# Kernel tuning notes

Hardware: AMD Instinct MI355X
Metric: run time of the kernel (lower is better)

The kernel has to match this reference:

```python
import jax, jax.numpy as jnp
import numpy as np

HIDDEN = 1024
INTER = 4096
N_EXPERTS = 8
TOP_K = 2


def setup_inputs() -> dict:
    key = jax.random.key(0)
    ks = jax.random.split(key, 5)
    B, S = 2, 1024
    scale_h = 1.0 / np.sqrt(HIDDEN)
    scale_i = 1.0 / np.sqrt(INTER)
    return {
        "hidden_states": jax.random.normal(ks[0], (B, S, HIDDEN), dtype=jnp.float32),
        "router_w": jax.random.normal(ks[1], (N_EXPERTS, HIDDEN), dtype=jnp.float32) * scale_h,
        "gate_w": jax.random.normal(ks[2], (N_EXPERTS, INTER, HIDDEN), dtype=jnp.float32) * scale_h,
        "up_w": jax.random.normal(ks[3], (N_EXPERTS, INTER, HIDDEN), dtype=jnp.float32) * scale_h,
        "down_w": jax.random.normal(ks[4], (N_EXPERTS, HIDDEN, INTER), dtype=jnp.float32) * scale_i,
        "top_k": TOP_K,
    }


def reference(hidden_states, router_w, gate_w, up_w, down_w, top_k):
    B, S, D = hidden_states.shape
    E = router_w.shape[0]
    x = hidden_states.reshape(-1, D)              # [T, D]
    T = x.shape[0]

    router_logits = x @ router_w.T                # [T, E]
    probs = jax.nn.softmax(router_logits.astype(jnp.float32), axis=-1)
    routing_weights, selected = jax.lax.top_k(probs, top_k)   # [T, k]
    routing_weights = routing_weights.astype(x.dtype)

    # Dense combine weights: w[t, e] = routing weight if expert e selected for token t else 0
    combine = jnp.zeros((T, E), x.dtype).at[jnp.arange(T)[:, None], selected].add(routing_weights)

    # SwiGLU expert MLPs, computed for all experts then combined (same math as gather/scatter loop)
    g = jnp.einsum('td,ehd->eth', x, gate_w)      # [E, T, H]
    u = jnp.einsum('td,ehd->eth', x, up_w)        # [E, T, H]
    h = jax.nn.silu(g) * u
    expert_out = jnp.einsum('eth,edh->etd', h, down_w)  # [E, T, D]
    out = jnp.einsum('etd,te->td', expert_out, combine)  # [T, D]

    return out.reshape(B, S, D), router_logits
```

## Files before the change

### kernel.cpp

```cpp
#include <hip/hip_runtime.h>
#include <hip/hip_bf16.h>

#define HIDDEN 1024
#define INTER 4096
#define NEXP 8
#define T_TOK 2048

typedef short bf16x8 __attribute__((ext_vector_type(8)));
typedef float f32x4 __attribute__((ext_vector_type(4)));

#define CHUNK(row, kq) ((unsigned int)((row) * 64u + ((((unsigned int)(kq)) ^ ((((unsigned int)(row)) >> 1) & 3u)) << 4)))

__device__ __forceinline__ unsigned short f2bf(float f) {
    union { float f; unsigned int u; } v; v.f = f;
    return (unsigned short)(v.u >> 16);
}

__device__ __forceinline__ uint4 pack8trunc(float4 a, float4 b) {
    union { float4 f; unsigned short s[8]; } x, y; x.f = a; y.f = b;
    uint4 r;
    r.x = (unsigned int)x.s[1] | ((unsigned int)x.s[3] << 16);
    r.y = (unsigned int)x.s[5] | ((unsigned int)x.s[7] << 16);
    r.z = (unsigned int)y.s[1] | ((unsigned int)y.s[3] << 16);
    r.w = (unsigned int)y.s[5] | ((unsigned int)y.s[7] << 16);
    return r;
}

__device__ __forceinline__ void block_sync() {
    asm volatile("s_waitcnt lgkmcnt(0)" ::: "memory");
    __builtin_amdgcn_s_barrier();
    asm volatile("" ::: "memory");
}

__global__ void router_kernel(const float* __restrict__ x,
                              const float* __restrict__ rw,
                              float* __restrict__ logits_out,
                              int* __restrict__ counts,
                              int* __restrict__ ids,
                              float* __restrict__ wts,
                              int* __restrict__ tsel) {
    int t = blockIdx.x * 4 + (threadIdx.x >> 6);
    int lane = threadIdx.x & 63;
    if (t >= T_TOK) return;
    const float4* xr = (const float4*)(x + (size_t)t * HIDDEN);
    float acc[NEXP];
#pragma unroll
    for (int e = 0; e < NEXP; e++) acc[e] = 0.f;
#pragma unroll
    for (int c = 0; c < 4; c++) {
        float4 xv = xr[lane + c * 64];
#pragma unroll
        for (int e = 0; e < NEXP; e++) {
            float4 wv = ((const float4*)(rw + (size_t)e * HIDDEN))[lane + c * 64];
            acc[e] += xv.x * wv.x + xv.y * wv.y + xv.z * wv.z + xv.w * wv.w;
        }
    }
#pragma unroll
    for (int e = 0; e < NEXP; e++) {
        float v = acc[e];
        for (int off = 32; off >= 1; off >>= 1) v += __shfl_xor(v, off, 64);
        acc[e] = v;
    }
    if (lane == 0) {
        float* lo = logits_out + (size_t)t * NEXP;
        float mx = acc[0];
#pragma unroll
        for (int e = 1; e < NEXP; e++) mx = fmaxf(mx, acc[e]);
        float p[NEXP], s = 0.f;
#pragma unroll
        for (int e = 0; e < NEXP; e++) { p[e] = __expf(acc[e] - mx); s += p[e]; }
        float inv = 1.f / s;
#pragma unroll
        for (int e = 0; e < NEXP; e++) { p[e] *= inv; lo[e] = acc[e]; }
        int i1 = 0;
#pragma unroll
        for (int e = 1; e < NEXP; e++) if (p[e] > p[i1]) i1 = e;
        int i2 = (i1 == 0) ? 1 : 0;
#pragma unroll
        for (int e = 0; e < NEXP; e++) if (e != i1 && e != i2 && p[e] > p[i2]) i2 = e;
        int s1 = atomicAdd(&counts[i1], 1);
        ids[i1 * T_TOK + s1] = t; wts[i1 * T_TOK + s1] = p[i1];
        int s2 = atomicAdd(&counts[i2], 1);
        ids[i2 * T_TOK + s2] = t; wts[i2 * T_TOK + s2] = p[i2];
        tsel[t * 2]     = i1 * T_TOK + s1;
        tsel[t * 2 + 1] = i2 * T_TOK + s2;
    }
}

__global__ void scan_kernel(const int* __restrict__ counts, int* __restrict__ offsets) {
    if (threadIdx.x == 0) {
        int s = 0;
        for (int e = 0; e < NEXP; e++) { offsets[e] = s; s += counts[e]; }
    }
}

__global__ __launch_bounds__(1024) void gemm_gu(
    const float* __restrict__ x, const float* __restrict__ gw, const float* __restrict__ uw,
    const int* __restrict__ counts, const int* __restrict__ offsets,
    const int* __restrict__ ids, unsigned short* __restrict__ h) {
    const int e = blockIdx.z;
    const int cnt = counts[e];
    const int mt = blockIdx.y;
    if (mt * 256 >= cnt) return;
    const int nt = blockIdx.x;
    const int tid = threadIdx.x;
    const int lane = tid & 63, wid = tid >> 6;
    const int wm = wid >> 2, wn = wid & 3;

    __shared__ __align__(16) char lds[65536];

    const int arow = tid >> 2, akq = tid & 3;
    int ali = mt * 256 + arow; if (ali >= cnt) ali = cnt - 1;
    const unsigned int aoff = (unsigned int)(ids[e * T_TOK + ali] * HIDDEN + akq * 8);
    const unsigned int wAo = CHUNK(arow, akq);
    const int bsel = tid >> 9;
    const int bi = tid & 511;
    const int brow = bi >> 2, bkq = bi & 3;
    const float* bsrc = (bsel ? uw : gw) + (size_t)e * INTER * HIDDEN
                        + (size_t)(nt * 128 + brow) * HIDDEN + bkq * 8;
    const unsigned int wBo = 16384u + ((unsigned int)bsel << 13) + CHUNK(brow, bkq);

    f32x4 accg[4][2], accu[4][2];
#pragma unroll
    for (int mf = 0; mf < 4; mf++)
#pragma unroll
        for (int nf = 0; nf < 2; nf++)
#pragma unroll
            for (int v = 0; v < 4; v++) { accg[mf][nf][v] = 0.f; accu[mf][nf][v] = 0.f; }

    float4 a0, a1, b0, b1;
    a0 = *(const float4*)(x + aoff); a1 = *(const float4*)(x + aoff + 4);
    b0 = *(const float4*)(bsrc);     b1 = *(const float4*)(bsrc + 4);

    for (int kt = 0; kt < 32; kt++) {
        const unsigned int bb = (unsigned int)(kt & 1) << 15;
        *(uint4*)(lds + bb + wAo) = pack8trunc(a0, a1);
        *(uint4*)(lds + bb + wBo) = pack8trunc(b0, b1);
        if (kt < 31) {
            const int ko = (kt + 1) * 32;
            a0 = *(const float4*)(x + aoff + ko); a1 = *(const float4*)(x + aoff + ko + 4);
            b0 = *(const float4*)(bsrc + ko);     b1 = *(const float4*)(bsrc + ko + 4);
        }
        block_sync();
        const unsigned int kqr = (unsigned int)(lane >> 4);
        const unsigned int rl = (unsigned int)(lane & 15);
        bf16x8 a[4];
#pragma unroll
        for (int mf = 0; mf < 4; mf++)
            a[mf] = *(const bf16x8*)(lds + bb + CHUNK(wm * 64 + mf * 16 + rl, kqr));
#pragma unroll
        for (int nf = 0; nf < 2; nf++) {
            const unsigned int br = wn * 32 + nf * 16 + rl;
            bf16x8 bg = *(const bf16x8*)(lds + bb + 16384 + CHUNK(br, kqr));
            bf16x8 bu = *(const bf16x8*)(lds + bb + 24576 + CHUNK(br, kqr));
#pragma unroll
            for (int mf = 0; mf < 4; mf++) {
                accg[mf][nf] = __builtin_amdgcn_mfma_f32_16x16x32_bf16(a[mf], bg, accg[mf][nf], 0, 0, 0);
                accu[mf][nf] = __builtin_amdgcn_mfma_f32_16x16x32_bf16(a[mf], bu, accu[mf][nf], 0, 0, 0);
            }
        }
    }

    const int hoff = offsets[e];
#pragma unroll
    for (int mf = 0; mf < 4; mf++)
#pragma unroll
        for (int v = 0; v < 4; v++) {
            int il = wm * 64 + mf * 16 + ((lane >> 4) << 2) + v;
            int i = mt * 256 + il;
            if (i < cnt) {
                size_t rowbase = (size_t)(hoff + i) * INTER + nt * 128 + wn * 32 + (lane & 15);
#pragma unroll
                for (int nf = 0; nf < 2; nf++) {
                    float g = accg[mf][nf][v], u = accu[mf][nf][v];
                    float sg = g / (1.f + __expf(-g));
                    h[rowbase + nf * 16] = f2bf(sg * u);
                }
            }
        }
}

__global__ __launch_bounds__(512) void gemm_down(
    const unsigned short* __restrict__ h, const float* __restrict__ dw,
    const int* __restrict__ counts, const int* __restrict__ offsets,
    const float* __restrict__ wts, float* __restrict__ y) {
    const int ez = blockIdx.z;
    const int e = ez >> 1, ksp = ez & 1;
    const int cnt = counts[e];
    const int mt = blockIdx.y;
    if (mt * 128 >= cnt) return;
    const int nt = blockIdx.x;
    const int tid = threadIdx.x;
    const int lane = tid & 63, wid = tid >> 6;
    const int wm = wid >> 2, wn = wid & 3;

    __shared__ __align__(16) char lds[32768];

    const int hoff = offsets[e];
    const float* dbase = dw + (size_t)e * HIDDEN * INTER;

    const int row = tid >> 2, kq = tid & 3;
    int li = mt * 128 + row; if (li >= cnt) li = cnt - 1;
    const unsigned int aoff = (unsigned int)((hoff + li) * INTER + ksp * 2048 + kq * 8);
    const unsigned int wAo = CHUNK(row, kq);
    const unsigned int boff = (unsigned int)((nt * 128 + row) * INTER + ksp * 2048 + kq * 8);
    const unsigned int wBo = 8192u + CHUNK(row, kq);

    f32x4 acc[4][2];
#pragma unroll
    for (int mf = 0; mf < 4; mf++)
#pragma unroll
        for (int nf = 0; nf < 2; nf++)
#pragma unroll
            for (int v = 0; v < 4; v++) acc[mf][nf][v] = 0.f;

    int4 av; float4 b0, b1;
    av = *(const int4*)(h + aoff);
    b0 = *(const float4*)(dbase + boff); b1 = *(const float4*)(dbase + boff + 4);

    for (int kt = 0; kt < 64; kt++) {
        const unsigned int bb = (unsigned int)(kt & 1) << 14;
        *(int4*)(lds + bb + wAo) = av;
        *(uint4*)(lds + bb + wBo) = pack8trunc(b0, b1);
        if (kt < 63) {
            const int ko = (kt + 1) * 32;
            av = *(const int4*)(h + aoff + ko);
            b0 = *(const float4*)(dbase + boff + ko); b1 = *(const float4*)(dbase + boff + ko + 4);
        }
        block_sync();
        const unsigned int kqr = (unsigned int)(lane >> 4);
        const unsigned int rl = (unsigned int)(lane & 15);
        bf16x8 a[4];
#pragma unroll
        for (int mf = 0; mf < 4; mf++)
            a[mf] = *(const bf16x8*)(lds + bb + CHUNK(wm * 64 + mf * 16 + rl, kqr));
#pragma unroll
        for (int nf = 0; nf < 2; nf++) {
            bf16x8 b = *(const bf16x8*)(lds + bb + 8192 + CHUNK(wn * 32 + nf * 16 + rl, kqr));
#pragma unroll
            for (int mf = 0; mf < 4; mf++)
                acc[mf][nf] = __builtin_amdgcn_mfma_f32_16x16x32_bf16(a[mf], b, acc[mf][nf], 0, 0, 0);
        }
    }

#pragma unroll
    for (int mf = 0; mf < 4; mf++)
#pragma unroll
        for (int v = 0; v < 4; v++) {
            int il = wm * 64 + mf * 16 + ((lane >> 4) << 2) + v;
            int i = mt * 128 + il;
            if (i < cnt) {
                float w = wts[e * T_TOK + i];
                float* yrow = y + ((size_t)ksp * 4096 + hoff + i) * HIDDEN
                                + nt * 128 + wn * 32 + (lane & 15);
#pragma unroll
                for (int nf = 0; nf < 2; nf++)
                    yrow[nf * 16] = w * acc[mf][nf][v];
            }
        }
}

__global__ __launch_bounds__(256) void combine_kernel(
    const float* __restrict__ y, const int* __restrict__ offsets,
    const int* __restrict__ tsel, float* __restrict__ out) {
    const int t = blockIdx.x;
    const int d = threadIdx.x * 4;
    int p0 = tsel[t * 2], p1 = tsel[t * 2 + 1];
    size_t g0 = (size_t)(offsets[p0 >> 11] + (p0 & (T_TOK - 1)));
    size_t g1 = (size_t)(offsets[p1 >> 11] + (p1 & (T_TOK - 1)));
    float4 a0 = *(const float4*)(y + g0 * HIDDEN + d);
    float4 a1 = *(const float4*)(y + (4096 + g0) * HIDDEN + d);
    float4 b0 = *(const float4*)(y + g1 * HIDDEN + d);
    float4 b1 = *(const float4*)(y + (4096 + g1) * HIDDEN + d);
    float4 o;
    o.x = (a0.x + a1.x) + (b0.x + b1.x);
    o.y = (a0.y + a1.y) + (b0.y + b1.y);
    o.z = (a0.z + a1.z) + (b0.z + b1.z);
    o.w = (a0.w + a1.w) + (b0.w + b1.w);
    *(float4*)(out + (size_t)t * HIDDEN + d) = o;
}

extern "C" void kernel_launch(void* const* d_in, const int* in_sizes, int n_in,
                              void* d_out, int out_size, void* d_ws, size_t ws_size,
                              hipStream_t stream) {
    const float* x  = (const float*)d_in[0];
    const float* rw = (const float*)d_in[1];
    const float* gw = (const float*)d_in[2];
    const float* uw = (const float*)d_in[3];
    const float* dw = (const float*)d_in[4];
    float* out = (float*)d_out;
    float* logits = out + (size_t)T_TOK * HIDDEN;

    char* ws = (char*)d_ws;
    int*   counts  = (int*)ws;
    int*   offsets = (int*)(ws + 32);
    int*   tsel    = (int*)(ws + 1024);
    int*   ids     = (int*)(ws + 20480);
    float* wts     = (float*)(ws + 90112);
    unsigned short* h = (unsigned short*)(ws + 262144);
    float* y       = (float*)(ws + 262144 + 33554432);

    hipMemsetAsync(counts, 0, 8 * sizeof(int), stream);

    router_kernel<<<T_TOK / 4, 256, 0, stream>>>(x, rw, logits, counts, ids, wts, tsel);
    scan_kernel<<<1, 64, 0, stream>>>(counts, offsets);
    gemm_gu<<<dim3(INTER / 128, 8, NEXP), 1024, 0, stream>>>(x, gw, uw, counts, offsets, ids, h);
    gemm_down<<<dim3(HIDDEN / 128, 16, NEXP * 2), 512, 0, stream>>>(h, dw, counts, offsets, wts, y);
    combine_kernel<<<T_TOK, 256, 0, stream>>>(y, offsets, tsel, out);
}
```

Before: 295.0 us.

## Restructure GEMM main loops into two-stage prefetch pipeline with split LDS buffers

Both the gate/up and down GEMM loops now stage the next tile into the alternate LDS buffer while computing on the current one, and prefetch global data two tiles ahead. The loop is unrolled by two with separate even/odd shared buffers, so buffer addresses are static. This is meant to hide global load latency and LDS write cost behind MFMA work. The barrier count per iteration stays at one. Register pressure rises somewhat and the extra prologue adds complexity.

```diff
diff --git a/kernel.cpp b/kernel.cpp
--- a/kernel.cpp
+++ b/kernel.cpp
@@ -107,7 +107,8 @@
     const int lane = tid & 63, wid = tid >> 6;
     const int wm = wid >> 2, wn = wid & 3;
 
-    __shared__ __align__(16) char lds[65536];
+    __shared__ __align__(16) char bufE[32768];
+    __shared__ __align__(16) char bufO[32768];
 
     const int arow = tid >> 2, akq = tid & 3;
     int ali = mt * 256 + arow; if (ali >= cnt) ali = cnt - 1;
@@ -128,38 +129,52 @@
 #pragma unroll
             for (int v = 0; v < 4; v++) { accg[mf][nf][v] = 0.f; accu[mf][nf][v] = 0.f; }
 
-    float4 a0, a1, b0, b1;
-    a0 = *(const float4*)(x + aoff); a1 = *(const float4*)(x + aoff + 4);
-    b0 = *(const float4*)(bsrc);     b1 = *(const float4*)(bsrc + 4);
-
-    for (int kt = 0; kt < 32; kt++) {
-        const unsigned int bb = (unsigned int)(kt & 1) << 15;
-        *(uint4*)(lds + bb + wAo) = pack8trunc(a0, a1);
-        *(uint4*)(lds + bb + wBo) = pack8trunc(b0, b1);
-        if (kt < 31) {
-            const int ko = (kt + 1) * 32;
-            a0 = *(const float4*)(x + aoff + ko); a1 = *(const float4*)(x + aoff + ko + 4);
-            b0 = *(const float4*)(bsrc + ko);     b1 = *(const float4*)(bsrc + ko + 4);
-        }
-        block_sync();
-        const unsigned int kqr = (unsigned int)(lane >> 4);
-        const unsigned int rl = (unsigned int)(lane & 15);
-        bf16x8 a[4];
-#pragma unroll
-        for (int mf = 0; mf < 4; mf++)
-            a[mf] = *(const bf16x8*)(lds + bb + CHUNK(wm * 64 + mf * 16 + rl, kqr));
-#pragma unroll
-        for (int nf = 0; nf < 2; nf++) {
-            const unsigned int br = wn * 32 + nf * 16 + rl;
-            bf16x8 bg = *(const bf16x8*)(lds + bb + 16384 + CHUNK(br, kqr));
-            bf16x8 bu = *(const bf16x8*)(lds + bb + 24576 + CHUNK(br, kqr));
-#pragma unroll
-            for (int mf = 0; mf < 4; mf++) {
-                accg[mf][nf] = __builtin_amdgcn_mfma_f32_16x16x32_bf16(a[mf], bg, accg[mf][nf], 0, 0, 0);
-                accu[mf][nf] = __builtin_amdgcn_mfma_f32_16x16x32_bf16(a[mf], bu, accu[mf][nf], 0, 0, 0);
-            }
-        }
-    }
+    float4 s0, s1, t0, t1;
+    s0 = *(const float4*)(x + aoff); s1 = *(const float4*)(x + aoff + 4);
+    t0 = *(const float4*)(bsrc);     t1 = *(const float4*)(bsrc + 4);
+    *(uint4*)(bufE + wAo) = pack8trunc(s0, s1);
+    *(uint4*)(bufE + wBo) = pack8trunc(t0, t1);
+    s0 = *(const float4*)(x + aoff + 32); s1 = *(const float4*)(x + aoff + 36);
+    t0 = *(const float4*)(bsrc + 32);     t1 = *(const float4*)(bsrc + 36);
+    block_sync();
+
+    const unsigned int kqr = (unsigned int)(lane >> 4);
+    const unsigned int rl = (unsigned int)(lane & 15);
+
+#define GU_BODY(KT, RB, WB)                                                             \
+    {                                                                                   \
+        bf16x8 fa[4];                                                                   \
+        _Pragma("unroll")                                                               \
+        for (int mf = 0; mf < 4; mf++)                                                  \
+            fa[mf] = *(const bf16x8*)((RB) + CHUNK(wm * 64 + mf * 16 + rl, kqr));       \
+        if ((KT) + 1 < 32) {                                                            \
+            *(uint4*)((WB) + wAo) = pack8trunc(s0, s1);                                 \
+            *(uint4*)((WB) + wBo) = pack8trunc(t0, t1);                                 \
+        }                                                                               \
+        if ((KT) + 2 < 32) {                                                            \
+            const int ko = ((KT) + 2) * 32;                                             \
+            s0 = *(const float4*)(x + aoff + ko); s1 = *(const float4*)(x + aoff + ko + 4); \
+            t0 = *(const float4*)(bsrc + ko);     t1 = *(const float4*)(bsrc + ko + 4); \
+        }                                                                               \
+        _Pragma("unroll")                                                               \
+        for (int nf = 0; nf < 2; nf++) {                                                \
+            const unsigned int br = wn * 32 + nf * 16 + rl;                             \
+            bf16x8 bg = *(const bf16x8*)((RB) + 16384 + CHUNK(br, kqr));                \
+            bf16x8 bu = *(const bf16x8*)((RB) + 24576 + CHUNK(br, kqr));                \
+            _Pragma("unroll")                                                           \
+            for (int mf = 0; mf < 4; mf++) {                                            \
+                accg[mf][nf] = __builtin_amdgcn_mfma_f32_16x16x32_bf16(fa[mf], bg, accg[mf][nf], 0, 0, 0); \
+                accu[mf][nf] = __builtin_amdgcn_mfma_f32_16x16x32_bf16(fa[mf], bu, accu[mf][nf], 0, 0, 0); \
+            }                                                                           \
+        }                                                                               \
+        block_sync();                                                                   \
+    }
+
+    for (int kt = 0; kt < 32; kt += 2) {
+        GU_BODY(kt, bufE, bufO)
+        GU_BODY(kt + 1, bufO, bufE)
+    }
+#undef GU_BODY
 
     const int hoff = offsets[e];
 #pragma unroll
@@ -194,7 +209,8 @@
     const int lane = tid & 63, wid = tid >> 6;
     const int wm = wid >> 2, wn = wid & 3;
 
-    __shared__ __align__(16) char lds[32768];
+    __shared__ __align__(16) char bufE[16384];
+    __shared__ __align__(16) char bufO[16384];
 
     const int hoff = offsets[e];
     const float* dbase = dw + (size_t)e * HIDDEN * INTER;
@@ -217,31 +233,45 @@
     int4 av; float4 b0, b1;
     av = *(const int4*)(h + aoff);
     b0 = *(const float4*)(dbase + boff); b1 = *(const float4*)(dbase + boff + 4);
-
-    for (int kt = 0; kt < 64; kt++) {
-        const unsigned int bb = (unsigned int)(kt & 1) << 14;
-        *(int4*)(lds + bb + wAo) = av;
-        *(uint4*)(lds + bb + wBo) = pack8trunc(b0, b1);
-        if (kt < 63) {
-            const int ko = (kt + 1) * 32;
-            av = *(const int4*)(h + aoff + ko);
-            b0 = *(const float4*)(dbase + boff + ko); b1 = *(const float4*)(dbase + boff + ko + 4);
-        }
-        block_sync();
-        const unsigned int kqr = (unsigned int)(lane >> 4);
-        const unsigned int rl = (unsigned int)(lane & 15);
-        bf16x8 a[4];
-#pragma unroll
-        for (int mf = 0; mf < 4; mf++)
-            a[mf] = *(const bf16x8*)(lds + bb + CHUNK(wm * 64 + mf * 16 + rl, kqr));
-#pragma unroll
-        for (int nf = 0; nf < 2; nf++) {
-            bf16x8 b = *(const bf16x8*)(lds + bb + 8192 + CHUNK(wn * 32 + nf * 16 + rl, kqr));
-#pragma unroll
-            for (int mf = 0; mf < 4; mf++)
-                acc[mf][nf] = __builtin_amdgcn_mfma_f32_16x16x32_bf16(a[mf], b, acc[mf][nf], 0, 0, 0);
-        }
-    }
+    *(int4*)(bufE + wAo) = av;
+    *(uint4*)(bufE + wBo) = pack8trunc(b0, b1);
+    av = *(const int4*)(h + aoff + 32);
+    b0 = *(const float4*)(dbase + boff + 32); b1 = *(const float4*)(dbase + boff + 36);
+    block_sync();
+
+    const unsigned int kqr = (unsigned int)(lane >> 4);
+    const unsigned int rl = (unsigned int)(lane & 15);
+
+#define DN_BODY(KT, RB, WB)                                                             \
+    {                                                                                   \
+        bf16x8 fa[4];                                                                   \
+        _Pragma("unroll")                                                               \
+        for (int mf = 0; mf < 4; mf++)                                                  \
+            fa[mf] = *(const bf16x8*)((RB) + CHUNK(wm * 64 + mf * 16 + rl, kqr));       \
+        if ((KT) + 1 < 64) {                                                            \
+            *(int4*)((WB) + wAo) = av;                                                  \
+            *(uint4*)((WB) + wBo) = pack8trunc(b0, b1);                                 \
+        }                                                                               \
+        if ((KT) + 2 < 64) {                                                            \
+            const int ko = ((KT) + 2) * 32;                                             \
+            av = *(const int4*)(h + aoff + ko);                                         \
+            b0 = *(const float4*)(dbase + boff + ko); b1 = *(const float4*)(dbase + boff + ko + 4); \
+        }                                                                               \
+        _Pragma("unroll")                                                               \
+        for (int nf = 0; nf < 2; nf++) {                                                \
+            bf16x8 b = *(const bf16x8*)((RB) + 8192 + CHUNK(wn * 32 + nf * 16 + rl, kqr)); \
+            _Pragma("unroll")                                                           \
+            for (int mf = 0; mf < 4; mf++)                                              \
+                acc[mf][nf] = __builtin_amdgcn_mfma_f32_16x16x32_bf16(fa[mf], b, acc[mf][nf], 0, 0, 0); \
+        }                                                                               \
+        block_sync();                                                                   \
+    }
+
+    for (int kt = 0; kt < 64; kt += 2) {
+        DN_BODY(kt, bufE, bufO)
+        DN_BODY(kt + 1, bufO, bufE)
+    }
+#undef DN_BODY
 
 #pragma unroll
     for (int mf = 0; mf < 4; mf++)
```

Result: no change. 294.2 us (-0.3%).

## Restructure gate/up GEMM into 512-thread, BK=64 four-phase pipelined mainloop

Applied to the files above, without the earlier changes.

The gate/up expert GEMM drops from 1024 to 512 threads. Each wave now covers 128 rows (8 M-fragments), and the K step grows from 32 to 64, held in a 128 KB double-buffered LDS with an XOR swizzle over 8 chunks. Each K tile is split into four phases that interleave LDS fragment reads, stores of the next tile, and global prefetch two phases ahead, with s_setprio raised around the MFMA bursts. The aim is to hide global-load latency and cut barrier and LDS overhead per MFMA, at the cost of more accumulator registers and much more LDS, which limits occupancy to one block per CU.

```diff
diff --git a/kernel.cpp b/kernel.cpp
--- a/kernel.cpp
+++ b/kernel.cpp
@@ -30,6 +30,16 @@
     asm volatile("s_waitcnt lgkmcnt(0)" ::: "memory");
     __builtin_amdgcn_s_barrier();
     asm volatile("" ::: "memory");
+}
+__device__ __forceinline__ void bar() {
+    asm volatile("" ::: "memory");
+    __builtin_amdgcn_s_barrier();
+    asm volatile("" ::: "memory");
+}
+__device__ __forceinline__ void bar_lgkm0() {
+    asm volatile("" ::: "memory");
+    __builtin_amdgcn_s_barrier();
+    asm volatile("s_waitcnt lgkmcnt(0)" ::: "memory");
 }
 
 __global__ void router_kernel(const float* __restrict__ x,
@@ -94,7 +104,7 @@
     }
 }
 
-__global__ __launch_bounds__(1024) void gemm_gu(
+__global__ __launch_bounds__(512) void gemm_gu(
     const float* __restrict__ x, const float* __restrict__ gw, const float* __restrict__ uw,
     const int* __restrict__ counts, const int* __restrict__ offsets,
     const int* __restrict__ ids, unsigned short* __restrict__ h) {
@@ -107,66 +117,161 @@
     const int lane = tid & 63, wid = tid >> 6;
     const int wm = wid >> 2, wn = wid & 3;
 
-    __shared__ __align__(16) char lds[65536];
-
-    const int arow = tid >> 2, akq = tid & 3;
-    int ali = mt * 256 + arow; if (ali >= cnt) ali = cnt - 1;
-    const unsigned int aoff = (unsigned int)(ids[e * T_TOK + ali] * HIDDEN + akq * 8);
-    const unsigned int wAo = CHUNK(arow, akq);
-    const int bsel = tid >> 9;
-    const int bi = tid & 511;
-    const int brow = bi >> 2, bkq = bi & 3;
-    const float* bsrc = (bsel ? uw : gw) + (size_t)e * INTER * HIDDEN
-                        + (size_t)(nt * 128 + brow) * HIDDEN + bkq * 8;
-    const unsigned int wBo = 16384u + ((unsigned int)bsel << 13) + CHUNK(brow, bkq);
-
-    f32x4 accg[4][2], accu[4][2];
-#pragma unroll
-    for (int mf = 0; mf < 4; mf++)
+    __shared__ __align__(16) char lds[131072];
+
+    const float* gbase = gw + (size_t)e * INTER * HIDDEN;
+    const float* ubase = uw + (size_t)e * INTER * HIDDEN;
+
+    const int r0 = tid >> 3;
+    const int kq = tid & 7;
+    unsigned int aoffs0, aoffs1, aoffs2, aoffs3;
+    {
+        int li, row;
+        row = r0;        li = mt * 256 + row; if (li >= cnt) li = cnt - 1;
+        aoffs0 = (unsigned int)(ids[e * T_TOK + li] * HIDDEN + kq * 8);
+        row = r0 + 64;   li = mt * 256 + row; if (li >= cnt) li = cnt - 1;
+        aoffs1 = (unsigned int)(ids[e * T_TOK + li] * HIDDEN + kq * 8);
+        row = r0 + 128;  li = mt * 256 + row; if (li >= cnt) li = cnt - 1;
+        aoffs2 = (unsigned int)(ids[e * T_TOK + li] * HIDDEN + kq * 8);
+        row = r0 + 192;  li = mt * 256 + row; if (li >= cnt) li = cnt - 1;
+        aoffs3 = (unsigned int)(ids[e * T_TOK + li] * HIDDEN + kq * 8);
+    }
+    const unsigned int boff0 = (unsigned int)((nt * 128 + r0) * HIDDEN + kq * 8);
+    const unsigned int boff1 = (unsigned int)((nt * 128 + r0 + 64) * HIDDEN + kq * 8);
+    const unsigned int kqs = (unsigned int)((kq ^ (r0 & 7)) << 4);
+    const unsigned int wA0 = (unsigned int)r0 * 128u + kqs;
+    const unsigned int wB0 = (unsigned int)r0 * 128u + kqs;
+
+    const unsigned int rl  = (unsigned int)(lane & 15);
+    const unsigned int kqr = (unsigned int)(lane >> 4);
+    const unsigned int fx  = rl & 7u;
+    const unsigned int aro = ((unsigned int)wm * 128u + rl) * 128u;
+    const unsigned int bro = ((unsigned int)wn * 32u + rl) * 128u;
+    const unsigned int kx0 = ((0u * 4u + kqr) ^ fx) << 4;
+    const unsigned int kx1 = ((1u * 4u + kqr) ^ fx) << 4;
+
+    f32x4 accg[8][2], accu[8][2];
+#pragma unroll
+    for (int mf = 0; mf < 8; mf++)
 #pragma unroll
         for (int nf = 0; nf < 2; nf++)
 #pragma unroll
             for (int v = 0; v < 4; v++) { accg[mf][nf][v] = 0.f; accu[mf][nf][v] = 0.f; }
 
-    float4 a0, a1, b0, b1;
-    a0 = *(const float4*)(x + aoff); a1 = *(const float4*)(x + aoff + 4);
-    b0 = *(const float4*)(bsrc);     b1 = *(const float4*)(bsrc + 4);
-
-    for (int kt = 0; kt < 32; kt++) {
-        const unsigned int bb = (unsigned int)(kt & 1) << 15;
-        *(uint4*)(lds + bb + wAo) = pack8trunc(a0, a1);
-        *(uint4*)(lds + bb + wBo) = pack8trunc(b0, b1);
-        if (kt < 31) {
-            const int ko = (kt + 1) * 32;
-            a0 = *(const float4*)(x + aoff + ko); a1 = *(const float4*)(x + aoff + ko + 4);
-            b0 = *(const float4*)(bsrc + ko);     b1 = *(const float4*)(bsrc + ko + 4);
-        }
-        block_sync();
-        const unsigned int kqr = (unsigned int)(lane >> 4);
-        const unsigned int rl = (unsigned int)(lane & 15);
-        bf16x8 a[4];
-#pragma unroll
-        for (int mf = 0; mf < 4; mf++)
-            a[mf] = *(const bf16x8*)(lds + bb + CHUNK(wm * 64 + mf * 16 + rl, kqr));
-#pragma unroll
-        for (int nf = 0; nf < 2; nf++) {
-            const unsigned int br = wn * 32 + nf * 16 + rl;
-            bf16x8 bg = *(const bf16x8*)(lds + bb + 16384 + CHUNK(br, kqr));
-            bf16x8 bu = *(const bf16x8*)(lds + bb + 24576 + CHUNK(br, kqr));
-#pragma unroll
-            for (int mf = 0; mf < 4; mf++) {
-                accg[mf][nf] = __builtin_amdgcn_mfma_f32_16x16x32_bf16(a[mf], bg, accg[mf][nf], 0, 0, 0);
-                accu[mf][nf] = __builtin_amdgcn_mfma_f32_16x16x32_bf16(a[mf], bu, accu[mf][nf], 0, 0, 0);
-            }
-        }
-    }
+    float4 s0a, s0b, s0c, s0d, s1a, s1b, s1c, s1d;
+
+    {
+        float4 pa, pb, pc, pd;
+        pa = *(const float4*)(x + aoffs0); pb = *(const float4*)(x + aoffs0 + 4);
+        pc = *(const float4*)(x + aoffs1); pd = *(const float4*)(x + aoffs1 + 4);
+        *(uint4*)(lds + wA0)         = pack8trunc(pa, pb);
+        *(uint4*)(lds + wA0 + 8192)  = pack8trunc(pc, pd);
+        pa = *(const float4*)(x + aoffs2); pb = *(const float4*)(x + aoffs2 + 4);
+        pc = *(const float4*)(x + aoffs3); pd = *(const float4*)(x + aoffs3 + 4);
+        *(uint4*)(lds + wA0 + 16384) = pack8trunc(pa, pb);
+        *(uint4*)(lds + wA0 + 24576) = pack8trunc(pc, pd);
+        pa = *(const float4*)(gbase + boff0); pb = *(const float4*)(gbase + boff0 + 4);
+        pc = *(const float4*)(gbase + boff1); pd = *(const float4*)(gbase + boff1 + 4);
+        *(uint4*)(lds + 32768 + wB0)        = pack8trunc(pa, pb);
+        *(uint4*)(lds + 32768 + wB0 + 8192) = pack8trunc(pc, pd);
+        pa = *(const float4*)(ubase + boff0); pb = *(const float4*)(ubase + boff0 + 4);
+        pc = *(const float4*)(ubase + boff1); pd = *(const float4*)(ubase + boff1 + 4);
+        *(uint4*)(lds + 49152 + wB0)        = pack8trunc(pa, pb);
+        *(uint4*)(lds + 49152 + wB0 + 8192) = pack8trunc(pc, pd);
+    }
+    s0a = *(const float4*)(x + aoffs0 + 64); s0b = *(const float4*)(x + aoffs0 + 68);
+    s0c = *(const float4*)(x + aoffs1 + 64); s0d = *(const float4*)(x + aoffs1 + 68);
+    s1a = *(const float4*)(x + aoffs2 + 64); s1b = *(const float4*)(x + aoffs2 + 68);
+    s1c = *(const float4*)(x + aoffs3 + 64); s1d = *(const float4*)(x + aoffs3 + 68);
+    block_sync();
+
+#define GU_MFMA16(HH, FA0, FA1, FA2, FA3)                                                    \
+    accg[(HH)*4+0][0] = __builtin_amdgcn_mfma_f32_16x16x32_bf16(FA0, bg0, accg[(HH)*4+0][0], 0, 0, 0); \
+    accg[(HH)*4+0][1] = __builtin_amdgcn_mfma_f32_16x16x32_bf16(FA0, bg1, accg[(HH)*4+0][1], 0, 0, 0); \
+    accu[(HH)*4+0][0] = __builtin_amdgcn_mfma_f32_16x16x32_bf16(FA0, bu0, accu[(HH)*4+0][0], 0, 0, 0); \
+    accu[(HH)*4+0][1] = __builtin_amdgcn_mfma_f32_16x16x32_bf16(FA0, bu1, accu[(HH)*4+0][1], 0, 0, 0); \
+    accg[(HH)*4+1][0] = __builtin_amdgcn_mfma_f32_16x16x32_bf16(FA1, bg0, accg[(HH)*4+1][0], 0, 0, 0); \
+    accg[(HH)*4+1][1] = __builtin_amdgcn_mfma_f32_16x16x32_bf16(FA1, bg1, accg[(HH)*4+1][1], 0, 0, 0); \
+    accu[(HH)*4+1][0] = __builtin_amdgcn_mfma_f32_16x16x32_bf16(FA1, bu0, accu[(HH)*4+1][0], 0, 0, 0); \
+    accu[(HH)*4+1][1] = __builtin_amdgcn_mfma_f32_16x16x32_bf16(FA1, bu1, accu[(HH)*4+1][1], 0, 0, 0); \
+    accg[(HH)*4+2][0] = __builtin_amdgcn_mfma_f32_16x16x32_bf16(FA2, bg0, accg[(HH)*4+2][0], 0, 0, 0); \
+    accg[(HH)*4+2][1] = __builtin_amdgcn_mfma_f32_16x16x32_bf16(FA2, bg1, accg[(HH)*4+2][1], 0, 0, 0); \
+    accu[(HH)*4+2][0] = __builtin_amdgcn_mfma_f32_16x16x32_bf16(FA2, bu0, accu[(HH)*4+2][0], 0, 0, 0); \
+    accu[(HH)*4+2][1] = __builtin_amdgcn_mfma_f32_16x16x32_bf16(FA2, bu1, accu[(HH)*4+2][1], 0, 0, 0); \
+    accg[(HH)*4+3][0] = __builtin_amdgcn_mfma_f32_16x16x32_bf16(FA3, bg0, accg[(HH)*4+3][0], 0, 0, 0); \
+    accg[(HH)*4+3][1] = __builtin_amdgcn_mfma_f32_16x16x32_bf16(FA3, bg1, accg[(HH)*4+3][1], 0, 0, 0); \
+    accu[(HH)*4+3][0] = __builtin_amdgcn_mfma_f32_16x16x32_bf16(FA3, bu0, accu[(HH)*4+3][0], 0, 0, 0); \
+    accu[(HH)*4+3][1] = __builtin_amdgcn_mfma_f32_16x16x32_bf16(FA3, bu1, accu[(HH)*4+3][1], 0, 0, 0);
+
+#define GU_PHASE(T, P, CB, NB, SA, SB, SC, SD)                                               \
+    {                                                                                        \
+        const unsigned int kxs = ((P) & 1) ? kx1 : kx0;                                      \
+        bf16x8 fa0 = *(const bf16x8*)(lds + (CB) + aro + (((P)>>1)*4+0)*2048 + kxs);         \
+        bf16x8 fa1 = *(const bf16x8*)(lds + (CB) + aro + (((P)>>1)*4+1)*2048 + kxs);         \
+        bf16x8 fa2 = *(const bf16x8*)(lds + (CB) + aro + (((P)>>1)*4+2)*2048 + kxs);         \
+        bf16x8 fa3 = *(const bf16x8*)(lds + (CB) + aro + (((P)>>1)*4+3)*2048 + kxs);         \
+        bf16x8 bg0 = *(const bf16x8*)(lds + (CB) + 32768 + bro + 0*2048 + kxs);              \
+        bf16x8 bg1 = *(const bf16x8*)(lds + (CB) + 32768 + bro + 1*2048 + kxs);              \
+        bf16x8 bu0 = *(const bf16x8*)(lds + (CB) + 49152 + bro + 0*2048 + kxs);              \
+        bf16x8 bu1 = *(const bf16x8*)(lds + (CB) + 49152 + bro + 1*2048 + kxs);              \
+        if ((T) < 15) {                                                                      \
+            if ((P) == 0) {                                                                  \
+                *(uint4*)(lds + (NB) + wA0)        = pack8trunc(SA, SB);                     \
+                *(uint4*)(lds + (NB) + wA0 + 8192) = pack8trunc(SC, SD);                     \
+            } else if ((P) == 1) {                                                           \
+                *(uint4*)(lds + (NB) + wA0 + 16384) = pack8trunc(SA, SB);                    \
+                *(uint4*)(lds + (NB) + wA0 + 24576) = pack8trunc(SC, SD);                    \
+            } else if ((P) == 2) {                                                           \
+                *(uint4*)(lds + (NB) + 32768 + wB0)        = pack8trunc(SA, SB);             \
+                *(uint4*)(lds + (NB) + 32768 + wB0 + 8192) = pack8trunc(SC, SD);             \
+            } else {                                                                         \
+                *(uint4*)(lds + (NB) + 49152 + wB0)        = pack8trunc(SA, SB);             \
+                *(uint4*)(lds + (NB) + 49152 + wB0 + 8192) = pack8trunc(SC, SD);             \
+            }                                                                                \
+        }                                                                                    \
+        {                                                                                    \
+            const int TL = (T) + 1 + (((P) + 2) >> 2);                                       \
+            if (TL < 16) {                                                                   \
+                const unsigned int ko = (unsigned int)TL * 64u;                              \
+                if ((((P) + 2) & 3) == 0) {                                                  \
+                    SA = *(const float4*)(x + aoffs0 + ko); SB = *(const float4*)(x + aoffs0 + ko + 4); \
+                    SC = *(const float4*)(x + aoffs1 + ko); SD = *(const float4*)(x + aoffs1 + ko + 4); \
+                } else if ((((P) + 2) & 3) == 1) {                                           \
+                    SA = *(const float4*)(x + aoffs2 + ko); SB = *(const float4*)(x + aoffs2 + ko + 4); \
+                    SC = *(const float4*)(x + aoffs3 + ko); SD = *(const float4*)(x + aoffs3 + ko + 4); \
+                } else if ((((P) + 2) & 3) == 2) {                                           \
+                    SA = *(const float4*)(gbase + boff0 + ko); SB = *(const float4*)(gbase + boff0 + ko + 4); \
+                    SC = *(const float4*)(gbase + boff1 + ko); SD = *(const float4*)(gbase + boff1 + ko + 4); \
+                } else {                                                                     \
+                    SA = *(const float4*)(ubase + boff0 + ko); SB = *(const float4*)(ubase + boff0 + ko + 4); \
+                    SC = *(const float4*)(ubase + boff1 + ko); SD = *(const float4*)(ubase + boff1 + ko + 4); \
+                }                                                                            \
+            }                                                                                \
+        }                                                                                    \
+        bar_lgkm0();                                                                         \
+        __builtin_amdgcn_s_setprio(1);                                                       \
+        GU_MFMA16((P) >> 1, fa0, fa1, fa2, fa3)                                              \
+        __builtin_amdgcn_s_setprio(0);                                                       \
+        bar();                                                                               \
+    }
+
+    for (int t = 0; t < 16; ++t) {
+        const unsigned int cb = (unsigned int)(t & 1) << 16;
+        const unsigned int nb = cb ^ 65536u;
+        GU_PHASE(t, 0, cb, nb, s0a, s0b, s0c, s0d)
+        GU_PHASE(t, 1, cb, nb, s1a, s1b, s1c, s1d)
+        GU_PHASE(t, 2, cb, nb, s0a, s0b, s0c, s0d)
+        GU_PHASE(t, 3, cb, nb, s1a, s1b, s1c, s1d)
+    }
+#undef GU_PHASE
+#undef GU_MFMA16
 
     const int hoff = offsets[e];
 #pragma unroll
-    for (int mf = 0; mf < 4; mf++)
+    for (int mf = 0; mf < 8; mf++)
 #pragma unroll
         for (int v = 0; v < 4; v++) {
-            int il = wm * 64 + mf * 16 + ((lane >> 4) << 2) + v;
+            int il = wm * 128 + mf * 16 + ((lane >> 4) << 2) + v;
             int i = mt * 256 + il;
             if (i < cnt) {
                 size_t rowbase = (size_t)(hoff + i) * INTER + nt * 128 + wn * 32 + (lane & 15);
@@ -304,7 +409,7 @@
 
     router_kernel<<<T_TOK / 4, 256, 0, stream>>>(x, rw, logits, counts, ids, wts, tsel);
     scan_kernel<<<1, 64, 0, stream>>>(counts, offsets);
-    gemm_gu<<<dim3(INTER / 128, 8, NEXP), 1024, 0, stream>>>(x, gw, uw, counts, offsets, ids, h);
+    gemm_gu<<<dim3(INTER / 128, 8, NEXP), 512, 0, stream>>>(x, gw, uw, counts, offsets, ids, h);
     gemm_down<<<dim3(HIDDEN / 128, 16, NEXP * 2), 512, 0, stream>>>(h, dw, counts, offsets, wts, y);
     combine_kernel<<<T_TOK, 256, 0, stream>>>(y, offsets, tsel, out);
 }
```

After: 312.5 us. 1.06x slower.
